# Optimization experiments

Measured on AMD Instinct MI355X. Metric: run time of the kernel, lower is better.

## Reference

```python
import jax, jax.numpy as jnp
import numpy as np

B, S, D, H = 8, 1024, 1024, 16  # batch, seq (queries==keys), d_model, heads
DH = D // H


def setup_inputs() -> dict:
    key = jax.random.key(0)
    ks = jax.random.split(key, 7)
    return {
        "query": jax.random.normal(ks[0], (B, S, D), dtype=jnp.float32),
        "key": jax.random.normal(ks[1], (B, S, D), dtype=jnp.float32),
        "value": jax.random.normal(ks[2], (B, S, D), dtype=jnp.float32),
        "valid_len": jax.random.randint(ks[3], (B, S), 0, S, dtype=jnp.int32),
        "Wq": jax.random.normal(ks[4], (D, D), dtype=jnp.float32) / np.sqrt(D),
        "Wk": jax.random.normal(ks[5], (D, D), dtype=jnp.float32) / np.sqrt(D),
        "Wv": jax.random.normal(ks[6], (D, D), dtype=jnp.float32) / np.sqrt(D),
    }


def reference(query, key, value, valid_len, Wq, Wk, Wv):
    b, sq, _ = query.shape
    sk = key.shape[1]
    # projections (bias-free Linear), then split hidden into H contiguous chunks per head
    q = (query @ Wq).reshape(b, sq, H, DH)  # [B,Sq,H,dh]
    k = (key @ Wk).reshape(b, sk, H, DH)
    v = (value @ Wv).reshape(b, sk, H, DH)
    scale = 1.0 / jnp.sqrt(jnp.asarray(DH, dtype=q.dtype))
    scores = jnp.einsum("bqhd,bkhd->bhqk", q, k) * scale  # [B,H,Sq,Sk]
    # per-query mask (valid_len.dim()==2 path): key index < valid_len[b, q]
    col = jnp.arange(sk)
    mask = col[None, None, None, :] < valid_len[:, None, :, None]  # [B,1,Sq,Sk]
    scores = jnp.where(mask, scores, jnp.asarray(-1000.0, dtype=scores.dtype))
    prob = jax.nn.softmax(scores, axis=-1)
    out = jnp.einsum("bhqk,bkhd->bqhd", prob, v)  # [B,Sq,H,dh]
    return out.reshape(b, sq, D)
```

## Files before the change

kernel.cpp:

```cpp
#include <hip/hip_runtime.h>
#include <hip/hip_bf16.h>
#include <stdint.h>


#define B_  8
#define S_  1024
#define D_  1024
#define H_  16
#define DH_ 64

typedef short bf16x8 __attribute__((ext_vector_type(8)));
typedef float f32x4  __attribute__((ext_vector_type(4)));
typedef unsigned short u16;
typedef uint32_t u32;
typedef u16 u16x8 __attribute__((ext_vector_type(8)));
typedef u16 u16x4 __attribute__((ext_vector_type(4)));

#define MASKVAL  (-1442.6950408889634f)
#define QSCALE   (0.18033688011112042f)

union U4 { u32 u[4]; bf16x8 v; };

__device__ __forceinline__ u16 f2bf(float f) {
    union { float f; uint32_t u; } v; v.f = f;
    uint32_t u = v.u;
    return (u16)((u + 0x7FFFu + ((u >> 16) & 1u)) >> 16);
}

__device__ __forceinline__ u32 cvtpk(float lo, float hi) {
    u32 r;
    asm("v_cvt_pk_bf16_f32 %0, %1, %2" : "=v"(r) : "v"(lo), "v"(hi));
    return r;
}

__device__ __forceinline__ void gload16(const void* g, const void* l) {
    __builtin_amdgcn_global_load_lds(
        (const __attribute__((address_space(1))) void*)g,
        (__attribute__((address_space(3))) void*)l, 16, 0, 0);
}

__device__ __forceinline__ float xor32max(float v) {
    float a = v, b = v;
    asm volatile("" : "+v"(b));
    asm("v_permlane32_swap_b32 %0, %1" : "+v"(a), "+v"(b));
    return fmaxf(a, b);
}
__device__ __forceinline__ float xor32add(float v) {
    float a = v, b = v;
    asm volatile("" : "+v"(b));
    asm("v_permlane32_swap_b32 %0, %1" : "+v"(a), "+v"(b));
    return a + b;
}

__global__ void transpose_w3_kernel(const float* __restrict__ Wq, const float* __restrict__ Wk,
                                    const float* __restrict__ Wv, u16* __restrict__ Wts) {
    __shared__ u16 tile[32 * 33];
    const int z = blockIdx.z;
    const float* W = (z == 0) ? Wq : (z == 1) ? Wk : Wv;
    u16* Wt = Wts + (size_t)z * D_ * D_;
    int k0 = blockIdx.y * 32, n0 = blockIdx.x * 32;
    int t = threadIdx.x;
    int c = t & 31;
    for (int p = 0; p < 4; ++p) {
        int r = p * 8 + (t >> 5);
        tile[r * 33 + c] = f2bf(W[(size_t)(k0 + r) * D_ + n0 + c]);
    }
    __syncthreads();
    int rn = t >> 3, c4 = t & 7;
    u16x4 v;
    for (int j = 0; j < 4; ++j) v[j] = tile[(c4 * 4 + j) * 33 + rn];
    *(u16x4*)(Wt + (size_t)(n0 + rn) * D_ + k0 + c4 * 4) = v;
}

__global__ __launch_bounds__(1024) void sort_vlen_kernel(const int* __restrict__ vlen,
                                                         int* __restrict__ qidx) {
    __shared__ u32 sk[1024];
    const int b = blockIdx.x, t = threadIdx.x;
    int k = vlen[b * S_ + t];
    u32 key = (k == 0) ? (u32)S_ : (u32)k;
    sk[t] = (key << 10) | (u32)t;
    __syncthreads();
    for (int sz = 2; sz <= 1024; sz <<= 1) {
        for (int st = sz >> 1; st > 0; st >>= 1) {
            int j = t ^ st;
            if (j > t) {
                u32 a = sk[t], c = sk[j];
                bool des = (t & sz) != 0;
                if ((a > c) != des) { sk[t] = c; sk[j] = a; }
            }
            __syncthreads();
        }
    }
    qidx[b * S_ + t] = (int)(sk[t] & 1023u);
}

__global__ __launch_bounds__(256) void gemm_qkv_kernel(const float* __restrict__ Aq,
                                                       const float* __restrict__ Ak,
                                                       const float* __restrict__ Av,
                                                       const u16* __restrict__ wts,
                                                       u16* __restrict__ qb, u16* __restrict__ kb,
                                                       u16* __restrict__ vb) {
    __shared__ float lds_a[2][128 * 32];
    __shared__ u16  lds_b[2][128 * 32];
    const int zy = blockIdx.y;
    const int z = zy >> 3;
    const float* A = (z == 0) ? Aq : (z == 1) ? Ak : Av;
    const u16* Bt = wts + (size_t)z * D_ * D_;
    u16* C = (z == 0) ? qb : (z == 1) ? kb : vb;
    const float cmul = (z == 0) ? QSCALE : 1.0f;

    const int t = threadIdx.x, w = t >> 6, l = t & 63;
    const int m0 = blockIdx.x * 128, n0 = (zy & 7) * 128;
    const int wr = w >> 1, wc = w & 1;
    const int l15 = l & 15, l4 = l >> 4;
    f32x4 acc[4][4] = {};

    auto stage = [&](int buf, int kt) {
        int k0 = kt * 32;
        #pragma unroll
        for (int i = 0; i < 4; ++i) {
            int c = i * 256 + t;
            int row = c >> 3, xs = (c & 7) ^ (row & 7);
            gload16(A + (size_t)(m0 + row) * D_ + k0 + xs * 4, &lds_a[buf][c * 4]);
        }
        #pragma unroll
        for (int i = 0; i < 2; ++i) {
            int c = i * 256 + t;
            int row = c >> 2, x = c & 3;
            gload16(Bt + (size_t)(n0 + row) * D_ + k0 + x * 8, &lds_b[buf][c * 8]);
        }
    };

    stage(0, 0);
    __syncthreads();
    int buf = 0;
    for (int kt = 0; kt < 32; ++kt) {
        if (kt + 1 < 32) stage(buf ^ 1, kt + 1);
        bf16x8 af[4], bfr[4];
        #pragma unroll
        for (int mi = 0; mi < 4; ++mi) {
            int r = wr * 64 + mi * 16 + l15;
            int c0 = (l4 * 2) ^ (r & 7), c1 = (l4 * 2 + 1) ^ (r & 7);
            float4 fa0 = *(const float4*)&lds_a[buf][r * 32 + c0 * 4];
            float4 fa1 = *(const float4*)&lds_a[buf][r * 32 + c1 * 4];
            U4 d;
            d.u[0] = cvtpk(fa0.x, fa0.y); d.u[1] = cvtpk(fa0.z, fa0.w);
            d.u[2] = cvtpk(fa1.x, fa1.y); d.u[3] = cvtpk(fa1.z, fa1.w);
            af[mi] = d.v;
        }
        #pragma unroll
        for (int ni = 0; ni < 4; ++ni)
            bfr[ni] = *(const bf16x8*)&lds_b[buf][(wc * 64 + ni * 16 + l15) * 32 + l4 * 8];
        #pragma unroll
        for (int mi = 0; mi < 4; ++mi)
            #pragma unroll
            for (int ni = 0; ni < 4; ++ni)
                acc[mi][ni] = __builtin_amdgcn_mfma_f32_16x16x32_bf16(af[mi], bfr[ni], acc[mi][ni], 0, 0, 0);
        __syncthreads();
        buf ^= 1;
    }
    #pragma unroll
    for (int mi = 0; mi < 4; ++mi)
        #pragma unroll
        for (int ni = 0; ni < 4; ++ni)
            #pragma unroll
            for (int r = 0; r < 4; ++r) {
                int m = m0 + wr * 64 + mi * 16 + l4 * 4 + r;
                int n = n0 + wc * 64 + ni * 16 + l15;
                C[(size_t)m * D_ + n] = f2bf(acc[mi][ni][r] * cmul);
            }
}

__global__ void transpose_v_kernel(const u16* __restrict__ vb, u16* __restrict__ vt) {
    __shared__ u16 t2[64 * 72];
    int bid = blockIdx.x;
    int st = bid & 15, bh = bid >> 4;
    int b = bh >> 4, h = bh & 15;
    int t = threadIdx.x;
    for (int p = 0; p < 2; ++p) {
        int c = p * 256 + t, r = c >> 3, x = c & 7;
        u16x8 val = *(const u16x8*)&vb[((size_t)(b * S_ + st * 64 + r)) * D_ + h * 64 + x * 8];
        *(u16x8*)&t2[r * 72 + x * 8] = val;
    }
    __syncthreads();
    int d = t >> 2, kc = t & 3;
    u16x8 o0, o1;
    for (int j = 0; j < 8; ++j) o0[j] = t2[(kc * 16 + j) * 72 + d];
    for (int j = 0; j < 8; ++j) o1[j] = t2[(kc * 16 + 8 + j) * 72 + d];
    size_t obase = ((size_t)bh * 64 + d) * (size_t)S_ + st * 64 + kc * 16;
    *(u16x8*)&vt[obase] = o0;
    *(u16x8*)&vt[obase + 8] = o1;
}

__global__ __launch_bounds__(512) void attn_kernel(const u16* __restrict__ qb,
                                                   const u16* __restrict__ kb,
                                                   const u16* __restrict__ vt,
                                                   const int* __restrict__ vlen,
                                                   const int* __restrict__ qidx,
                                                   float* __restrict__ out) {
    __shared__ __align__(16) char smem_raw[34816];
    auto kv = [&](int buf, int which) -> u16* {
        return (u16*)(smem_raw + buf * 16384 + which * 8192);
    };

    const int t = threadIdx.x, w = t >> 6, l = t & 63;
    const int n = blockIdx.x;
    const int x = n & 7, j = n >> 3;
    const int bh = x + 8 * (j >> 2);
    const int p = j & 3;
    const int b = bh >> 4, h = bh & 15;
    const int l15 = l & 15, l4 = l >> 4;
    const bool rowe = ((l & 16) == 0);

    const u16* kbase = kb + ((size_t)(b * S_)) * D_ + h * 64;
    const u16* vbase = vt + ((size_t)bh * 64) * (size_t)S_;

    const int kr_s = t >> 3, x_s = (t & 7) ^ (kr_s & 7);
    auto stage = [&](int buf, int kt) {
        gload16(kbase + (size_t)(kt * 64 + kr_s) * D_ + x_s * 8, &kv(buf, 0)[t * 8]);
        gload16(vbase + (size_t)kr_s * S_ + kt * 64 + x_s * 8, &kv(buf, 1)[t * 8]);
    };

    auto redist = [&](u32 P, u32 Q, u32& oe, u32& oo) {
        u32 X = P, Y = Q;
        asm("v_permlane32_swap_b32 %0, %1" : "+v"(X), "+v"(Y));
        u32 t1 = (u32)__shfl_xor((int)Y, 16, 64);
        u32 t2 = (u32)__shfl_xor((int)X, 16, 64);
        oe = rowe ? X : t1;
        oo = rowe ? t2 : Y;
    };

    for (int jb = 0; jb < 2; ++jb) {
        const int qblk = (jb == 0) ? (7 - p) : p;
        const int q0 = qblk * 128;

        const int qi = qidx[b * S_ + q0 + w * 16 + l15];
        const u16* qptr = qb + ((size_t)(b * S_ + qi)) * D_ + h * 64 + l4 * 8;
        const bf16x8 bq0 = *(const bf16x8*)qptr;
        const bf16x8 bq1 = *(const bf16x8*)(qptr + 32);
        const int vlq = vlen[b * S_ + qi];

        int mk = vlen[b * S_ + qidx[b * S_ + q0 + 127]];
        if (mk == 0) mk = S_;
        const int nkt = (mk + 63) >> 6;

        int vm = (vlq == 0) ? S_ : vlq;
        {
            int s1 = __shfl_xor(vm, 1, 64);  vm = vm > s1 ? vm : s1;
            int s2 = __shfl_xor(vm, 2, 64);  vm = vm > s2 ? vm : s2;
            int s4 = __shfl_xor(vm, 4, 64);  vm = vm > s4 ? vm : s4;
            int s8 = __shfl_xor(vm, 8, 64);  vm = vm > s8 ? vm : s8;
        }
        const int nktw = (vm + 63) >> 6;

        float m = -3.0e38f, lsum = 0.f;
        f32x4 acc[4] = {};

        stage(0, 0);
        __syncthreads();

        int buf = 0;
        for (int kt = 0; kt < nkt; ++kt) {
            if (kt + 1 < nkt) stage(buf ^ 1, kt + 1);

            if (kt < nktw) {
                f32x4 sc[4];
                __builtin_amdgcn_s_setprio(1);
                #pragma unroll
                for (int nf = 0; nf < 4; ++nf) {
                    int kr = nf * 16 + l15, swz = kr & 7;
                    bf16x8 ak0 = *(const bf16x8*)&kv(buf, 0)[kr * 64 + ((l4 ^ swz) * 8)];
                    bf16x8 ak1 = *(const bf16x8*)&kv(buf, 0)[kr * 64 + (((l4 + 4) ^ swz) * 8)];
                    f32x4 s = {0.f, 0.f, 0.f, 0.f};
                    s = __builtin_amdgcn_mfma_f32_16x16x32_bf16(ak0, bq0, s, 0, 0, 0);
                    s = __builtin_amdgcn_mfma_f32_16x16x32_bf16(ak1, bq1, s, 0, 0, 0);
                    sc[nf] = s;
                }
                __builtin_amdgcn_s_setprio(0);

                const int thr = vlq - kt * 64 - 4 * l4;
                float pv[16];
                float pm = -3.0e38f;
                if (__all(thr >= 52)) {
                    #pragma unroll
                    for (int nf = 0; nf < 4; ++nf)
                        #pragma unroll
                        for (int r = 0; r < 4; ++r) {
                            float y = sc[nf][r];
                            pv[nf * 4 + r] = y;
                            pm = fmaxf(pm, y);
                        }
                } else {
                    #pragma unroll
                    for (int nf = 0; nf < 4; ++nf)
                        #pragma unroll
                        for (int r = 0; r < 4; ++r) {
                            float y = ((nf * 16 + r) < thr) ? sc[nf][r] : MASKVAL;
                            pv[nf * 4 + r] = y;
                            pm = fmaxf(pm, y);
                        }
                }
                pm = fmaxf(pm, __shfl_xor(pm, 16, 64));
                pm = xor32max(pm);
                if (!__all(pm - m <= 8.0f)) {
                    float mn = fmaxf(m, pm);
                    float corr = __builtin_amdgcn_exp2f(m - mn);
                    m = mn;
                    lsum *= corr;
                    #pragma unroll
                    for (int df = 0; df < 4; ++df) acc[df] *= corr;
                }
                float rs = 0.f;
                #pragma unroll
                for (int i = 0; i < 16; ++i) {
                    float e = __builtin_amdgcn_exp2f(pv[i] - m);
                    pv[i] = e;
                    rs += e;
                }
                rs += __shfl_xor(rs, 16, 64);
                rs = xor32add(rs);
                lsum += rs;

                u32 pw[8];
                #pragma unroll
                for (int nf = 0; nf < 4; ++nf) {
                    pw[2 * nf]     = cvtpk(pv[4 * nf + 0], pv[4 * nf + 1]);
                    pw[2 * nf + 1] = cvtpk(pv[4 * nf + 2], pv[4 * nf + 3]);
                }
                U4 pb0, pb1;
                redist(pw[0], pw[2], pb0.u[0], pb0.u[2]);
                redist(pw[1], pw[3], pb0.u[1], pb0.u[3]);
                redist(pw[4], pw[6], pb1.u[0], pb1.u[2]);
                redist(pw[5], pw[7], pb1.u[1], pb1.u[3]);

                __builtin_amdgcn_s_setprio(1);
                #pragma unroll
                for (int df = 0; df < 4; ++df) {
                    int vr = df * 16 + l15, swz = vr & 7;
                    bf16x8 av0 = *(const bf16x8*)&kv(buf, 1)[vr * 64 + ((l4 ^ swz) * 8)];
                    bf16x8 av1 = *(const bf16x8*)&kv(buf, 1)[vr * 64 + (((l4 + 4) ^ swz) * 8)];
                    acc[df] = __builtin_amdgcn_mfma_f32_16x16x32_bf16(av0, pb0.v, acc[df], 0, 0, 0);
                    acc[df] = __builtin_amdgcn_mfma_f32_16x16x32_bf16(av1, pb1.v, acc[df], 0, 0, 0);
                }
                __builtin_amdgcn_s_setprio(0);
            }

            __syncthreads();
            buf ^= 1;
        }

        const float inv = 1.0f / lsum;
        __syncthreads();
        float* ep = (float*)smem_raw;
        #pragma unroll
        for (int df = 0; df < 4; ++df)
            #pragma unroll
            for (int r = 0; r < 4; ++r)
                ep[w * 1088 + l15 * 68 + df * 16 + 4 * l4 + r] = acc[df][r] * inv;
        __syncthreads();
        #pragma unroll
        for (int rr = 0; rr < 4; ++rr) {
            int row = l4 * 4 + rr;
            int qi2 = qidx[b * S_ + q0 + w * 16 + row];
            float4 vv = *(float4*)&ep[w * 1088 + row * 68 + l15 * 4];
            *(float4*)&out[((size_t)(b * S_ + qi2)) * D_ + h * 64 + l15 * 4] = vv;
        }
        __syncthreads();
    }
}

extern "C" void kernel_launch(void* const* d_in, const int* in_sizes, int n_in,
                              void* d_out, int out_size, void* d_ws, size_t ws_size,
                              hipStream_t stream) {
    const float* query = (const float*)d_in[0];
    const float* key   = (const float*)d_in[1];
    const float* value = (const float*)d_in[2];
    const int*   vlen  = (const int*)d_in[3];
    const float* Wq    = (const float*)d_in[4];
    const float* Wk    = (const float*)d_in[5];
    const float* Wv    = (const float*)d_in[6];
    float* out = (float*)d_out;

    char* ws = (char*)d_ws;
    const size_t MB = 1024 * 1024;
    const size_t TSZ = (size_t)B_ * S_ * D_ * 2;
    u16* wts = (u16*)(ws);
    u16* vt  = (u16*)(ws + 6 * MB);
    u16* qb  = (u16*)(ws + 6 * MB + TSZ);
    u16* kb  = (u16*)(ws + 6 * MB + 2 * TSZ);
    u16* vb  = (u16*)(ws + 6 * MB + 3 * TSZ);
    int* qidx = (int*)(ws + 6 * MB + 4 * TSZ);

    dim3 blk(256);

    transpose_w3_kernel<<<dim3(32, 32, 3), blk, 0, stream>>>(Wq, Wk, Wv, wts);
    sort_vlen_kernel<<<B_, dim3(1024), 0, stream>>>(vlen, qidx);

    gemm_qkv_kernel<<<dim3(64, 24), blk, 0, stream>>>(query, key, value, wts, qb, kb, vb);

    transpose_v_kernel<<<B_ * H_ * (S_ / 64), blk, 0, stream>>>(vb, vt);

    attn_kernel<<<dim3(512), dim3(512), 0, stream>>>(qb, kb, vt, vlen, qidx, out);
}
```

Before: 150.3 us.

## Process both query blocks in one K/V pass and swizzle GEMM B tile in LDS

```diff
diff --git a/kernel.cpp b/kernel.cpp
--- a/kernel.cpp
+++ b/kernel.cpp
@@ -126,8 +126,8 @@
         #pragma unroll
         for (int i = 0; i < 2; ++i) {
             int c = i * 256 + t;
-            int row = c >> 2, x = c & 3;
-            gload16(Bt + (size_t)(n0 + row) * D_ + k0 + x * 8, &lds_b[buf][c * 8]);
+            int row = c >> 2, xc = (c & 3) ^ (row & 3);
+            gload16(Bt + (size_t)(n0 + row) * D_ + k0 + xc * 8, &lds_b[buf][c * 8]);
         }
     };
 
@@ -149,8 +149,10 @@
             af[mi] = d.v;
         }
         #pragma unroll
-        for (int ni = 0; ni < 4; ++ni)
-            bfr[ni] = *(const bf16x8*)&lds_b[buf][(wc * 64 + ni * 16 + l15) * 32 + l4 * 8];
+        for (int ni = 0; ni < 4; ++ni) {
+            int r = wc * 64 + ni * 16 + l15;
+            bfr[ni] = *(const bf16x8*)&lds_b[buf][r * 32 + ((l4 ^ (r & 3)) * 8)];
+        }
         #pragma unroll
         for (int mi = 0; mi < 4; ++mi)
             #pragma unroll
@@ -230,142 +232,166 @@
         oo = rowe ? t2 : Y;
     };
 
-    for (int jb = 0; jb < 2; ++jb) {
-        const int qblk = (jb == 0) ? (7 - p) : p;
-        const int q0 = qblk * 128;
-
-        const int qi = qidx[b * S_ + q0 + w * 16 + l15];
-        const u16* qptr = qb + ((size_t)(b * S_ + qi)) * D_ + h * 64 + l4 * 8;
-        const bf16x8 bq0 = *(const bf16x8*)qptr;
-        const bf16x8 bq1 = *(const bf16x8*)(qptr + 32);
-        const int vlq = vlen[b * S_ + qi];
-
-        int mk = vlen[b * S_ + qidx[b * S_ + q0 + 127]];
-        if (mk == 0) mk = S_;
-        const int nkt = (mk + 63) >> 6;
-
-        int vm = (vlq == 0) ? S_ : vlq;
-        {
-            int s1 = __shfl_xor(vm, 1, 64);  vm = vm > s1 ? vm : s1;
-            int s2 = __shfl_xor(vm, 2, 64);  vm = vm > s2 ? vm : s2;
-            int s4 = __shfl_xor(vm, 4, 64);  vm = vm > s4 ? vm : s4;
-            int s8 = __shfl_xor(vm, 8, 64);  vm = vm > s8 ? vm : s8;
-        }
-        const int nktw = (vm + 63) >> 6;
-
-        float m = -3.0e38f, lsum = 0.f;
-        f32x4 acc[4] = {};
-
-        stage(0, 0);
+    auto wavemax = [&](int v) {
+        int s1 = __shfl_xor(v, 1, 64);  v = v > s1 ? v : s1;
+        int s2 = __shfl_xor(v, 2, 64);  v = v > s2 ? v : s2;
+        int s4 = __shfl_xor(v, 4, 64);  v = v > s4 ? v : s4;
+        int s8 = __shfl_xor(v, 8, 64);  v = v > s8 ? v : s8;
+        return v;
+    };
+
+    const int q0a = (7 - p) * 128, q0b = p * 128;
+
+    const int qia = qidx[b * S_ + q0a + w * 16 + l15];
+    const u16* qpa = qb + ((size_t)(b * S_ + qia)) * D_ + h * 64 + l4 * 8;
+    const bf16x8 bqa0 = *(const bf16x8*)qpa;
+    const bf16x8 bqa1 = *(const bf16x8*)(qpa + 32);
+    const int vla = vlen[b * S_ + qia];
+
+    const int qib = qidx[b * S_ + q0b + w * 16 + l15];
+    const u16* qpb = qb + ((size_t)(b * S_ + qib)) * D_ + h * 64 + l4 * 8;
+    const bf16x8 bqb0 = *(const bf16x8*)qpb;
+    const bf16x8 bqb1 = *(const bf16x8*)(qpb + 32);
+    const int vlb = vlen[b * S_ + qib];
+
+    int mk = vlen[b * S_ + qidx[b * S_ + q0a + 127]];
+    if (mk == 0) mk = S_;
+    const int nkt = (mk + 63) >> 6;
+
+    const int nktwa = (wavemax(vla == 0 ? S_ : vla) + 63) >> 6;
+    const int nktwb = (wavemax(vlb == 0 ? S_ : vlb) + 63) >> 6;
+
+    float ma = -3.0e38f, lsa = 0.f, mb = -3.0e38f, lsb = 0.f;
+    f32x4 acca[4] = {}, accb[4] = {};
+
+    auto process = [&](int buf, int kt, const bf16x8& bq0, const bf16x8& bq1, int vlq,
+                       float& m, float& lsum, f32x4 (&acc)[4]) {
+        f32x4 sc[4];
+        __builtin_amdgcn_s_setprio(1);
+        #pragma unroll
+        for (int nf = 0; nf < 4; ++nf) {
+            int kr = nf * 16 + l15, swz = kr & 7;
+            bf16x8 ak0 = *(const bf16x8*)&kv(buf, 0)[kr * 64 + ((l4 ^ swz) * 8)];
+            bf16x8 ak1 = *(const bf16x8*)&kv(buf, 0)[kr * 64 + (((l4 + 4) ^ swz) * 8)];
+            f32x4 s = {0.f, 0.f, 0.f, 0.f};
+            s = __builtin_amdgcn_mfma_f32_16x16x32_bf16(ak0, bq0, s, 0, 0, 0);
+            s = __builtin_amdgcn_mfma_f32_16x16x32_bf16(ak1, bq1, s, 0, 0, 0);
+            sc[nf] = s;
+        }
+        __builtin_amdgcn_s_setprio(0);
+
+        const int thr = vlq - kt * 64 - 4 * l4;
+        float pv[16];
+        float pm = -3.0e38f;
+        if (__all(thr >= 52)) {
+            #pragma unroll
+            for (int nf = 0; nf < 4; ++nf)
+                #pragma unroll
+                for (int r = 0; r < 4; ++r) {
+                    float y = sc[nf][r];
+                    pv[nf * 4 + r] = y;
+                    pm = fmaxf(pm, y);
+                }
+        } else {
+            #pragma unroll
+            for (int nf = 0; nf < 4; ++nf)
+                #pragma unroll
+                for (int r = 0; r < 4; ++r) {
+                    float y = ((nf * 16 + r) < thr) ? sc[nf][r] : MASKVAL;
+                    pv[nf * 4 + r] = y;
+                    pm = fmaxf(pm, y);
+                }
+        }
+        pm = fmaxf(pm, __shfl_xor(pm, 16, 64));
+        pm = xor32max(pm);
+        if (!__all(pm - m <= 8.0f)) {
+            float mn = fmaxf(m, pm);
+            float corr = __builtin_amdgcn_exp2f(m - mn);
+            m = mn;
+            lsum *= corr;
+            #pragma unroll
+            for (int df = 0; df < 4; ++df) acc[df] *= corr;
+        }
+        float rs = 0.f;
+        #pragma unroll
+        for (int i = 0; i < 16; ++i) {
+            float e = __builtin_amdgcn_exp2f(pv[i] - m);
+            pv[i] = e;
+            rs += e;
+        }
+        rs += __shfl_xor(rs, 16, 64);
+        rs = xor32add(rs);
+        lsum += rs;
+
+        u32 pw[8];
+        #pragma unroll
+        for (int nf = 0; nf < 4; ++nf) {
+            pw[2 * nf]     = cvtpk(pv[4 * nf + 0], pv[4 * nf + 1]);
+            pw[2 * nf + 1] = cvtpk(pv[4 * nf + 2], pv[4 * nf + 3]);
+        }
+        U4 pb0, pb1;
+        redist(pw[0], pw[2], pb0.u[0], pb0.u[2]);
+        redist(pw[1], pw[3], pb0.u[1], pb0.u[3]);
+        redist(pw[4], pw[6], pb1.u[0], pb1.u[2]);
+        redist(pw[5], pw[7], pb1.u[1], pb1.u[3]);
+
+        __builtin_amdgcn_s_setprio(1);
+        #pragma unroll
+        for (int df = 0; df < 4; ++df) {
+            int vr = df * 16 + l15, swz = vr & 7;
+            bf16x8 av0 = *(const bf16x8*)&kv(buf, 1)[vr * 64 + ((l4 ^ swz) * 8)];
+            bf16x8 av1 = *(const bf16x8*)&kv(buf, 1)[vr * 64 + (((l4 + 4) ^ swz) * 8)];
+            acc[df] = __builtin_amdgcn_mfma_f32_16x16x32_bf16(av0, pb0.v, acc[df], 0, 0, 0);
+            acc[df] = __builtin_amdgcn_mfma_f32_16x16x32_bf16(av1, pb1.v, acc[df], 0, 0, 0);
+        }
+        __builtin_amdgcn_s_setprio(0);
+    };
+
+    stage(0, 0);
+    __syncthreads();
+
+    int buf = 0;
+    for (int kt = 0; kt < nkt; ++kt) {
+        if (kt + 1 < nkt) stage(buf ^ 1, kt + 1);
+        if (kt < nktwa) process(buf, kt, bqa0, bqa1, vla, ma, lsa, acca);
+        if (kt < nktwb) process(buf, kt, bqb0, bqb1, vlb, mb, lsb, accb);
         __syncthreads();
-
-        int buf = 0;
-        for (int kt = 0; kt < nkt; ++kt) {
-            if (kt + 1 < nkt) stage(buf ^ 1, kt + 1);
-
-            if (kt < nktw) {
-                f32x4 sc[4];
-                __builtin_amdgcn_s_setprio(1);
-                #pragma unroll
-                for (int nf = 0; nf < 4; ++nf) {
-                    int kr = nf * 16 + l15, swz = kr & 7;
-                    bf16x8 ak0 = *(const bf16x8*)&kv(buf, 0)[kr * 64 + ((l4 ^ swz) * 8)];
-                    bf16x8 ak1 = *(const bf16x8*)&kv(buf, 0)[kr * 64 + (((l4 + 4) ^ swz) * 8)];
-                    f32x4 s = {0.f, 0.f, 0.f, 0.f};
-                    s = __builtin_amdgcn_mfma_f32_16x16x32_bf16(ak0, bq0, s, 0, 0, 0);
-                    s = __builtin_amdgcn_mfma_f32_16x16x32_bf16(ak1, bq1, s, 0, 0, 0);
-                    sc[nf] = s;
-                }
-                __builtin_amdgcn_s_setprio(0);
-
-                const int thr = vlq - kt * 64 - 4 * l4;
-                float pv[16];
-                float pm = -3.0e38f;
-                if (__all(thr >= 52)) {
-                    #pragma unroll
-                    for (int nf = 0; nf < 4; ++nf)
-                        #pragma unroll
-                        for (int r = 0; r < 4; ++r) {
-                            float y = sc[nf][r];
-                            pv[nf * 4 + r] = y;
-                            pm = fmaxf(pm, y);
-                        }
-                } else {
-                    #pragma unroll
-                    for (int nf = 0; nf < 4; ++nf)
-                        #pragma unroll
-                        for (int r = 0; r < 4; ++r) {
-                            float y = ((nf * 16 + r) < thr) ? sc[nf][r] : MASKVAL;
-                            pv[nf * 4 + r] = y;
-                            pm = fmaxf(pm, y);
-                        }
-                }
-                pm = fmaxf(pm, __shfl_xor(pm, 16, 64));
-                pm = xor32max(pm);
-                if (!__all(pm - m <= 8.0f)) {
-                    float mn = fmaxf(m, pm);
-                    float corr = __builtin_amdgcn_exp2f(m - mn);
-                    m = mn;
-                    lsum *= corr;
-                    #pragma unroll
-                    for (int df = 0; df < 4; ++df) acc[df] *= corr;
-                }
-                float rs = 0.f;
-                #pragma unroll
-                for (int i = 0; i < 16; ++i) {
-                    float e = __builtin_amdgcn_exp2f(pv[i] - m);
-                    pv[i] = e;
-                    rs += e;
-                }
-                rs += __shfl_xor(rs, 16, 64);
-                rs = xor32add(rs);
-                lsum += rs;
-
-                u32 pw[8];
-                #pragma unroll
-                for (int nf = 0; nf < 4; ++nf) {
-                    pw[2 * nf]     = cvtpk(pv[4 * nf + 0], pv[4 * nf + 1]);
-                    pw[2 * nf + 1] = cvtpk(pv[4 * nf + 2], pv[4 * nf + 3]);
-                }
-                U4 pb0, pb1;
-                redist(pw[0], pw[2], pb0.u[0], pb0.u[2]);
-                redist(pw[1], pw[3], pb0.u[1], pb0.u[3]);
-                redist(pw[4], pw[6], pb1.u[0], pb1.u[2]);
-                redist(pw[5], pw[7], pb1.u[1], pb1.u[3]);
-
-                __builtin_amdgcn_s_setprio(1);
-                #pragma unroll
-                for (int df = 0; df < 4; ++df) {
-                    int vr = df * 16 + l15, swz = vr & 7;
-                    bf16x8 av0 = *(const bf16x8*)&kv(buf, 1)[vr * 64 + ((l4 ^ swz) * 8)];
-                    bf16x8 av1 = *(const bf16x8*)&kv(buf, 1)[vr * 64 + (((l4 + 4) ^ swz) * 8)];
-                    acc[df] = __builtin_amdgcn_mfma_f32_16x16x32_bf16(av0, pb0.v, acc[df], 0, 0, 0);
-                    acc[df] = __builtin_amdgcn_mfma_f32_16x16x32_bf16(av1, pb1.v, acc[df], 0, 0, 0);
-                }
-                __builtin_amdgcn_s_setprio(0);
-            }
-
-            __syncthreads();
-            buf ^= 1;
-        }
-
-        const float inv = 1.0f / lsum;
-        __syncthreads();
-        float* ep = (float*)smem_raw;
+        buf ^= 1;
+    }
+
+    float* ep = (float*)smem_raw;
+    {
+        const float inv = 1.0f / lsa;
         #pragma unroll
         for (int df = 0; df < 4; ++df)
             #pragma unroll
             for (int r = 0; r < 4; ++r)
-                ep[w * 1088 + l15 * 68 + df * 16 + 4 * l4 + r] = acc[df][r] * inv;
+                ep[w * 1088 + l15 * 68 + df * 16 + 4 * l4 + r] = acca[df][r] * inv;
         __syncthreads();
         #pragma unroll
         for (int rr = 0; rr < 4; ++rr) {
             int row = l4 * 4 + rr;
-            int qi2 = qidx[b * S_ + q0 + w * 16 + row];
+            int qi2 = qidx[b * S_ + q0a + w * 16 + row];
             float4 vv = *(float4*)&ep[w * 1088 + row * 68 + l15 * 4];
             *(float4*)&out[((size_t)(b * S_ + qi2)) * D_ + h * 64 + l15 * 4] = vv;
         }
         __syncthreads();
+    }
+    {
+        const float inv = 1.0f / lsb;
+        #pragma unroll
+        for (int df = 0; df < 4; ++df)
+            #pragma unroll
+            for (int r = 0; r < 4; ++r)
+                ep[w * 1088 + l15 * 68 + df * 16 + 4 * l4 + r] = accb[df][r] * inv;
+        __syncthreads();
+        #pragma unroll
+        for (int rr = 0; rr < 4; ++rr) {
+            int row = l4 * 4 + rr;
+            int qi2 = qidx[b * S_ + q0b + w * 16 + row];
+            float4 vv = *(float4*)&ep[w * 1088 + row * 68 + l15 * 4];
+            *(float4*)&out[((size_t)(b * S_ + qi2)) * D_ + h * 64 + l15 * 4] = vv;
+        }
     }
 }
 
```

Result: slower. 163.9 us (+9.0%).
